# Optimization experiments

Hardware: AMD Instinct MI355X
Metric: run time of the kernel (lower is better)

The kernel has to match this reference:

```python
import jax, jax.numpy as jnp
import numpy as np

EPS = 1e-5

def _layernorm(x, g, b):
    mu = jnp.mean(x, axis=-1, keepdims=True)
    var = jnp.mean(jnp.square(x - mu), axis=-1, keepdims=True)
    return (x - mu) * jax.lax.rsqrt(var + EPS) * g + b

def _silu(x):
    return x * jax.nn.sigmoid(x)

def _xavier(key, shape):
    fan_out, fan_in = shape
    limit = np.sqrt(6.0 / (fan_in + fan_out))
    return jax.random.uniform(key, shape, jnp.float32, -limit, limit)

def setup_inputs() -> dict:
    key = jax.random.key(0)
    ks = jax.random.split(key, 4)
    B = 2097152
    return {
        'x': jax.random.normal(ks[0], (B, 24), jnp.float32),
        'w1': _xavier(ks[1], (64, 24)), 'b1': jnp.zeros((64,), jnp.float32),
        'g1': jnp.ones((64,), jnp.float32), 'be1': jnp.zeros((64,), jnp.float32),
        'w2': _xavier(ks[2], (64, 64)), 'b2': jnp.zeros((64,), jnp.float32),
        'g2': jnp.ones((64,), jnp.float32), 'be2': jnp.zeros((64,), jnp.float32),
        'w3': _xavier(ks[3], (7, 64)), 'b3': jnp.zeros((7,), jnp.float32),
        'g3': jnp.ones((7,), jnp.float32), 'be3': jnp.zeros((7,), jnp.float32),
    }

def reference(x, w1, b1, g1, be1, w2, b2, g2, be2, w3, b3, g3, be3):
    h = _silu(_layernorm(x @ w1.T + b1, g1, be1))      # [B, 64]
    h = _silu(_layernorm(h @ w2.T + b2, g2, be2))      # [B, 64]
    h = _layernorm(h @ w3.T + b3, g3, be3)             # [B, 7]
    return jax.nn.softmax(h, axis=-1)
```

## Files before the change

kernel.cpp:

```cpp
#include <hip/hip_runtime.h>
#include <math.h>

#define BLOCK 256
#define WPB 4
#define NBLOCKS 2048

typedef float  f32x4 __attribute__((ext_vector_type(4)));
typedef float  f32x2 __attribute__((ext_vector_type(2)));
typedef short  short8 __attribute__((ext_vector_type(8)));
typedef unsigned int u32;
typedef u32 u32x4 __attribute__((ext_vector_type(4)));
typedef u32 u32x2 __attribute__((ext_vector_type(2)));

static __device__ __forceinline__ f32x4 mfma16(short8 a, short8 b, f32x4 c) {
    return __builtin_amdgcn_mfma_f32_16x16x32_bf16(a, b, c, 0, 0, 0);
}

static __device__ __forceinline__ f32x4 zero4() { f32x4 z = {0.f, 0.f, 0.f, 0.f}; return z; }

static __device__ __forceinline__ u32 cvt_pk(float lo, float hi) {
    u32 r;
    asm("v_cvt_pk_bf16_f32 %0, %1, %2" : "=v"(r) : "v"(lo), "v"(hi));
    return r;
}
static __device__ __forceinline__ float unpk_lo(u32 p) { return __builtin_bit_cast(float, p << 16); }
static __device__ __forceinline__ float unpk_hi(u32 p) { return __builtin_bit_cast(float, p & 0xffff0000u); }

static __device__ __forceinline__ short8 mk_frag(u32 a, u32 b, u32 c, u32 d) {
    u32x4 t = {a, b, c, d};
    return __builtin_bit_cast(short8, t);
}

struct Frag2 { short8 hi, lo; };

static __device__ __forceinline__ Frag2 split8(f32x4 a, f32x4 b) {
    u32 h0 = cvt_pk(a[0], a[1]), h1 = cvt_pk(a[2], a[3]);
    u32 h2 = cvt_pk(b[0], b[1]), h3 = cvt_pk(b[2], b[3]);
    u32 l0 = cvt_pk(a[0] - unpk_lo(h0), a[1] - unpk_hi(h0));
    u32 l1 = cvt_pk(a[2] - unpk_lo(h1), a[3] - unpk_hi(h1));
    u32 l2 = cvt_pk(b[0] - unpk_lo(h2), b[1] - unpk_hi(h2));
    u32 l3 = cvt_pk(b[2] - unpk_lo(h3), b[3] - unpk_hi(h3));
    Frag2 r; r.hi = mk_frag(h0, h1, h2, h3); r.lo = mk_frag(l0, l1, l2, l3);
    return r;
}

static __device__ __forceinline__ void split4(f32x4 v, u32x2& hi, u32x2& lo) {
    u32 h0 = cvt_pk(v[0], v[1]), h1 = cvt_pk(v[2], v[3]);
    u32 l0 = cvt_pk(v[0] - unpk_lo(h0), v[1] - unpk_hi(h0));
    u32 l1 = cvt_pk(v[2] - unpk_lo(h1), v[3] - unpk_hi(h1));
    hi = u32x2{h0, h1}; lo = u32x2{l0, l1};
}

static __device__ __forceinline__ Frag2 wfrag(const float* p) {
    return split8(*(const f32x4*)p, *(const f32x4*)(p + 4));
}

static __device__ __forceinline__ float red4(float v) {
    v += __shfl_xor(v, 16);
    v += __shfl_xor(v, 32);
    return v;
}
static __device__ __forceinline__ float redmax4(float v) {
    v = fmaxf(v, __shfl_xor(v, 16));
    v = fmaxf(v, __shfl_xor(v, 32));
    return v;
}

struct TState {
    f32x4 xa, xb;
    f32x4 d[4];
    short8 bhHi[2], bhLo[2];
    f32x4 d3;
};

static __device__ __forceinline__ void ph_l1(TState& t, const Frag2& bx, const Frag2* w1f) {
#pragma unroll
    for (int mt = 0; mt < 4; ++mt) {
        f32x4 d = mfma16(w1f[mt].hi, bx.hi, zero4());
        d = mfma16(w1f[mt].hi, bx.lo, d);
        d = mfma16(w1f[mt].lo, bx.hi, d);
        t.d[mt] = d;
    }
}

static __device__ __forceinline__ void ph_l2_lds(TState& t,
        const unsigned char* sW2h, const unsigned char* sW2l, u32 crow, u32 ch, int q) {
    const u32 r0 = crow + ((((u32)q) ^ ch) << 4);
    const u32 r1 = crow + ((((u32)(4 + q)) ^ ch) << 4);
#pragma unroll
    for (int mt = 0; mt < 4; ++mt) {
        const u32 mo = (u32)mt * 2048u;
        short8 h0 = *(const short8*)(sW2h + mo + r0);
        short8 h1 = *(const short8*)(sW2h + mo + r1);
        short8 l0 = *(const short8*)(sW2l + mo + r0);
        short8 l1 = *(const short8*)(sW2l + mo + r1);
        f32x4 d = mfma16(h0, t.bhHi[0], zero4());
        d = mfma16(h0, t.bhLo[0], d);
        d = mfma16(l0, t.bhHi[0], d);
        d = mfma16(h1, t.bhHi[1], d);
        d = mfma16(h1, t.bhLo[1], d);
        d = mfma16(l1, t.bhHi[1], d);
        t.d[mt] = d;
    }
}

static __device__ __forceinline__ void ph_l3(TState& t, const Frag2* w3f) {
    f32x4 a = mfma16(w3f[0].hi, t.bhHi[0], zero4());
    a = mfma16(w3f[0].hi, t.bhLo[0], a);
    a = mfma16(w3f[0].lo, t.bhHi[0], a);
    f32x4 b = mfma16(w3f[1].hi, t.bhHi[1], zero4());
    b = mfma16(w3f[1].hi, t.bhLo[1], b);
    b = mfma16(w3f[1].lo, t.bhHi[1], b);
#pragma unroll
    for (int r = 0; r < 4; ++r) t.d3[r] = a[r] + b[r];
}

template<int PB, int PG, int PBE>
static __device__ __forceinline__ void ph_ln_silu(TState& t, const float* sP, int q) {
    float s = 0.f, s2 = 0.f;
#pragma unroll
    for (int mt = 0; mt < 4; ++mt) {
        if (PB >= 0) {
            const f32x4 bv = *(const f32x4*)(sP + PB + mt * 16 + q * 4);
#pragma unroll
            for (int r = 0; r < 4; ++r) t.d[mt][r] += bv[r];
        }
#pragma unroll
        for (int r = 0; r < 4; ++r) { float v = t.d[mt][r]; s += v; s2 = fmaf(v, v, s2); }
    }
    s = red4(s); s2 = red4(s2);
    const float mu = s * (1.f / 64.f);
    const float var = s2 * (1.f / 64.f) - mu * mu;
    const float inv = __builtin_amdgcn_rsqf(var + 1e-5f);
    const float cns = -mu * inv;
#pragma unroll
    for (int mt = 0; mt < 4; ++mt) {
        const f32x4 gv  = *(const f32x4*)(sP + PG  + mt * 16 + q * 4);
        const f32x4 bev = *(const f32x4*)(sP + PBE + mt * 16 + q * 4);
#pragma unroll
        for (int r = 0; r < 4; ++r) {
            float tt = fmaf(t.d[mt][r], inv, cns);
            float v  = fmaf(tt, gv[r], bev[r]);
            t.d[mt][r] = v * __builtin_amdgcn_rcpf(1.f + __expf(-v));
        }
    }
}

static __device__ __forceinline__ void ph_stage(TState& t, unsigned char* sHi, unsigned char* sLo,
                                                u32 crow, u32 ch, int q) {
#pragma unroll
    for (int mt = 0; mt < 4; ++mt) {
        u32x2 hi, lo;
        split4(t.d[mt], hi, lo);
        u32 off = crow + ((((u32)(mt * 2 + (q >> 1))) ^ ch) << 4) + (u32)((q & 1) * 8);
        *(u32x2*)(sHi + off) = hi;
        *(u32x2*)(sLo + off) = lo;
    }
#pragma unroll
    for (int kk = 0; kk < 2; ++kk) {
        u32 roff = crow + ((((u32)(kk * 4 + q)) ^ ch) << 4);
        t.bhHi[kk] = *(const short8*)(sHi + roff);
        t.bhLo[kk] = *(const short8*)(sLo + roff);
    }
}

static __device__ __forceinline__ void ph_out(TState& t, const float* sP, int q, int c, int lane,
                                              unsigned char* ob, float* out, int tile,
                                              int oc0, int of0, int oc1, int of1) {
    const f32x4 b3v  = *(const f32x4*)(sP + 384 + q * 4);
    const f32x4 g3v  = *(const f32x4*)(sP + 400 + q * 4);
    const f32x4 be3v = *(const f32x4*)(sP + 416 + q * 4);
    f32x4 d3 = t.d3;
    float s = 0.f, s2 = 0.f;
#pragma unroll
    for (int r = 0; r < 4; ++r) {
        float v = d3[r] + b3v[r];
        d3[r] = v;
        const bool ok = (q * 4 + r) < 7;
        if (ok) { s += v; s2 = fmaf(v, v, s2); }
    }
    s = red4(s); s2 = red4(s2);
    const float mu = s * (1.f / 7.f);
    const float var = s2 * (1.f / 7.f) - mu * mu;
    const float inv = __builtin_amdgcn_rsqf(var + 1e-5f);
    const float cns = -mu * inv;

    float z[4]; float mx = -1e30f;
#pragma unroll
    for (int r = 0; r < 4; ++r) {
        z[r] = fmaf(fmaf(d3[r], inv, cns), g3v[r], be3v[r]);
        const bool ok = (q * 4 + r) < 7;
        if (ok) mx = fmaxf(mx, z[r]);
    }
    mx = redmax4(mx);
    float es = 0.f; float e[4];
#pragma unroll
    for (int r = 0; r < 4; ++r) {
        const bool ok = (q * 4 + r) < 7;
        e[r] = ok ? __expf(z[r] - mx) : 0.f;
        es += e[r];
    }
    es = red4(es);
    const float rs = __builtin_amdgcn_rcpf(es);

    if (q == 0) {
        f32x4 v = {e[0] * rs, e[1] * rs, e[2] * rs, e[3] * rs};
        *(f32x4*)(ob + c * 48) = v;
    } else if (q == 1) {
        f32x2 v = {e[0] * rs, e[1] * rs};
        *(f32x2*)(ob + c * 48 + 16) = v;
        *(float*)(ob + c * 48 + 24) = e[2] * rs;
    }
    float* outp = out + (size_t)tile * 112;
    outp[lane] = *(const float*)(ob + oc0 * 48 + of0 * 4);
    if (lane < 48) outp[64 + lane] = *(const float*)(ob + oc1 * 48 + of1 * 4);
}

__global__ __launch_bounds__(BLOCK, 3) void mlp_mfma4_kernel(
    const float* __restrict__ x,
    const float* __restrict__ w1, const float* __restrict__ b1,
    const float* __restrict__ g1, const float* __restrict__ be1,
    const float* __restrict__ w2, const float* __restrict__ b2,
    const float* __restrict__ g2, const float* __restrict__ be2,
    const float* __restrict__ w3, const float* __restrict__ b3,
    const float* __restrict__ g3, const float* __restrict__ be3,
    float* __restrict__ out, int ntiles)
{
    __shared__ __align__(16) unsigned char smem[WPB * 4096 + 16384];
    __shared__ __align__(16) float sP[6 * 64 + 3 * 16];

    const int tid = threadIdx.x;
    const int lane = tid & 63;
    const int wib  = tid >> 6;
    const int c = lane & 15;
    const int q = lane >> 4;

    unsigned char* wb   = smem + wib * 4096;
    unsigned char* sHi  = wb;
    unsigned char* sLo  = wb + 2048;
    unsigned char* ob   = sHi;
    unsigned char* sW2h = smem + WPB * 4096;
    unsigned char* sW2l = sW2h + 8192;

    for (int i = tid; i < 512; i += BLOCK) {
        const int row = i >> 3, cb = i & 7;
        Frag2 f = wfrag(w2 + row * 64 + cb * 8);
        const u32 off = (u32)row * 128u + (u32)((cb ^ (row & 7)) << 4);
        *(short8*)(sW2h + off) = f.hi;
        *(short8*)(sW2l + off) = f.lo;
    }
    if (tid < 64) {
        sP[        tid] = b1[tid];  sP[ 64 + tid] = g1[tid];  sP[128 + tid] = be1[tid];
        sP[192 + tid] = b2[tid];    sP[256 + tid] = g2[tid];  sP[320 + tid] = be2[tid];
    }
    if (tid < 16) {
        const bool ok = tid < 7;
        sP[384 + tid] = ok ? b3[tid]  : 0.f;
        sP[400 + tid] = ok ? g3[tid]  : 0.f;
        sP[416 + tid] = ok ? be3[tid] : 0.f;
    }

    const u32 crow = (u32)c * 128u;
    const u32 ch   = (u32)(c & 7);

    Frag2 w1f[4];
#pragma unroll
    for (int mt = 0; mt < 4; ++mt) {
        if (q < 3) {
            w1f[mt] = wfrag(w1 + (mt * 16 + c) * 24 + q * 8);
        } else {
            float s = b1[mt * 16 + c];
            f32x4 a = {s, 0.f, 0.f, 0.f};
            w1f[mt] = split8(a, zero4());
        }
    }
    Frag2 w3f[2];
#pragma unroll
    for (int kk = 0; kk < 2; ++kk) {
        if (c < 7) w3f[kk] = wfrag(w3 + c * 64 + kk * 32 + q * 8);
        else       { w3f[kk].hi = mk_frag(0,0,0,0); w3f[kk].lo = mk_frag(0,0,0,0); }
    }

    __syncthreads();

    const int oc0 = lane / 7, of0 = lane - oc0 * 7;
    const int i1 = lane + 64;
    const int oc1 = i1 / 7, of1 = i1 - oc1 * 7;

    const int wid = blockIdx.x * WPB + wib;
    const int ts  = gridDim.x * WPB;

    TState A;
    A.xa = zero4(); A.xb = zero4();
    if (wid < ntiles && q < 3) {
        const float* xp = x + ((size_t)wid * 16 + c) * 24 + q * 8;
        A.xa = *(const f32x4*)xp; A.xb = *(const f32x4*)(xp + 4);
    }
    if (q == 3) A.xa[0] = 1.0f;

    for (int tile = wid; tile < ntiles; tile += ts) {
        asm volatile("" ::: "memory");

        Frag2 bx = split8(A.xa, A.xb);

        {
            const int nt = tile + ts;
            if (nt < ntiles && q < 3) {
                const float* xp = x + ((size_t)nt * 16 + c) * 24 + q * 8;
                A.xa = *(const f32x4*)xp; A.xb = *(const f32x4*)(xp + 4);
            }
        }

        ph_l1(A, bx, w1f);
        ph_ln_silu<-1, 64, 128>(A, sP, q);
        ph_stage(A, sHi, sLo, crow, ch, q);
        ph_l2_lds(A, sW2h, sW2l, crow, ch, q);
        ph_ln_silu<192, 256, 320>(A, sP, q);
        ph_stage(A, sHi, sLo, crow, ch, q);
        ph_l3(A, w3f);
        ph_out(A, sP, q, c, lane, ob, out, tile, oc0, of0, oc1, of1);
    }
}

extern "C" void kernel_launch(void* const* d_in, const int* in_sizes, int n_in,
                              void* d_out, int out_size, void* d_ws, size_t ws_size,
                              hipStream_t stream) {
    const float* x   = (const float*)d_in[0];
    const float* w1  = (const float*)d_in[1];
    const float* b1  = (const float*)d_in[2];
    const float* g1  = (const float*)d_in[3];
    const float* be1 = (const float*)d_in[4];
    const float* w2  = (const float*)d_in[5];
    const float* b2  = (const float*)d_in[6];
    const float* g2  = (const float*)d_in[7];
    const float* be2 = (const float*)d_in[8];
    const float* w3  = (const float*)d_in[9];
    const float* b3  = (const float*)d_in[10];
    const float* g3  = (const float*)d_in[11];
    const float* be3 = (const float*)d_in[12];
    float* out = (float*)d_out;

    const int B = in_sizes[0] / 24;
    const int ntiles = B / 16;
    hipLaunchKernelGGL(mlp_mfma4_kernel, dim3(NBLOCKS), dim3(BLOCK), 0, stream,
                       x, w1, b1, g1, be1, w2, b2, g2, be2, w3, b3, g3, be3,
                       out, ntiles);
}
```

Before: 190.0 us.

## Move W3 fragments to LDS and raise occupancy target to four blocks per CU

The layer-3 weight fragments were held in registers for the whole persistent loop. They are now stored in a swizzled LDS buffer and reloaded every tile, which frees VGPRs so the launch bound can go from 3 to 4 blocks per CU. The LayerNorm and softmax math is also rewritten as vector f32x4 operations with a tree reduction. The cost is extra LDS reads per tile and 4 KB more shared memory per block, and forcing the tighter register budget could cause spills.

```diff
diff --git a/kernel.cpp b/kernel.cpp
--- a/kernel.cpp
+++ b/kernel.cpp
@@ -104,30 +104,37 @@
     }
 }
 
-static __device__ __forceinline__ void ph_l3(TState& t, const Frag2* w3f) {
-    f32x4 a = mfma16(w3f[0].hi, t.bhHi[0], zero4());
-    a = mfma16(w3f[0].hi, t.bhLo[0], a);
-    a = mfma16(w3f[0].lo, t.bhHi[0], a);
-    f32x4 b = mfma16(w3f[1].hi, t.bhHi[1], zero4());
-    b = mfma16(w3f[1].hi, t.bhLo[1], b);
-    b = mfma16(w3f[1].lo, t.bhHi[1], b);
-#pragma unroll
-    for (int r = 0; r < 4; ++r) t.d3[r] = a[r] + b[r];
+static __device__ __forceinline__ void ph_l3_lds(TState& t,
+        const unsigned char* sW3h, const unsigned char* sW3l, u32 crow, u32 ch, int q) {
+    const u32 r0 = crow + ((((u32)q) ^ ch) << 4);
+    const u32 r1 = crow + ((((u32)(4 + q)) ^ ch) << 4);
+    short8 h0 = *(const short8*)(sW3h + r0);
+    short8 h1 = *(const short8*)(sW3h + r1);
+    short8 l0 = *(const short8*)(sW3l + r0);
+    short8 l1 = *(const short8*)(sW3l + r1);
+    f32x4 a = mfma16(h0, t.bhHi[0], zero4());
+    a = mfma16(h0, t.bhLo[0], a);
+    a = mfma16(l0, t.bhHi[0], a);
+    f32x4 b = mfma16(h1, t.bhHi[1], zero4());
+    b = mfma16(h1, t.bhLo[1], b);
+    b = mfma16(l1, t.bhHi[1], b);
+    t.d3 = a + b;
 }
 
 template<int PB, int PG, int PBE>
 static __device__ __forceinline__ void ph_ln_silu(TState& t, const float* sP, int q) {
-    float s = 0.f, s2 = 0.f;
-#pragma unroll
-    for (int mt = 0; mt < 4; ++mt) {
-        if (PB >= 0) {
-            const f32x4 bv = *(const f32x4*)(sP + PB + mt * 16 + q * 4);
-#pragma unroll
-            for (int r = 0; r < 4; ++r) t.d[mt][r] += bv[r];
-        }
-#pragma unroll
-        for (int r = 0; r < 4; ++r) { float v = t.d[mt][r]; s += v; s2 = fmaf(v, v, s2); }
-    }
+    if (PB >= 0) {
+#pragma unroll
+        for (int mt = 0; mt < 4; ++mt)
+            t.d[mt] += *(const f32x4*)(sP + PB + mt * 16 + q * 4);
+    }
+    f32x4 acc  = (t.d[0] + t.d[1]) + (t.d[2] + t.d[3]);
+    f32x4 acc2 = t.d[0] * t.d[0];
+    acc2 += t.d[1] * t.d[1];
+    acc2 += t.d[2] * t.d[2];
+    acc2 += t.d[3] * t.d[3];
+    float s  = (acc[0] + acc[1]) + (acc[2] + acc[3]);
+    float s2 = (acc2[0] + acc2[1]) + (acc2[2] + acc2[3]);
     s = red4(s); s2 = red4(s2);
     const float mu = s * (1.f / 64.f);
     const float var = s2 * (1.f / 64.f) - mu * mu;
@@ -137,12 +144,13 @@
     for (int mt = 0; mt < 4; ++mt) {
         const f32x4 gv  = *(const f32x4*)(sP + PG  + mt * 16 + q * 4);
         const f32x4 bev = *(const f32x4*)(sP + PBE + mt * 16 + q * 4);
-#pragma unroll
-        for (int r = 0; r < 4; ++r) {
-            float tt = fmaf(t.d[mt][r], inv, cns);
-            float v  = fmaf(tt, gv[r], bev[r]);
-            t.d[mt][r] = v * __builtin_amdgcn_rcpf(1.f + __expf(-v));
-        }
+        f32x4 tt = t.d[mt] * inv + cns;
+        f32x4 v  = tt * gv + bev;
+        f32x4 sg;
+#pragma unroll
+        for (int r = 0; r < 4; ++r)
+            sg[r] = __builtin_amdgcn_rcpf(1.f + __expf(-v[r]));
+        t.d[mt] = v * sg;
     }
 }
 
@@ -170,14 +178,12 @@
     const f32x4 b3v  = *(const f32x4*)(sP + 384 + q * 4);
     const f32x4 g3v  = *(const f32x4*)(sP + 400 + q * 4);
     const f32x4 be3v = *(const f32x4*)(sP + 416 + q * 4);
-    f32x4 d3 = t.d3;
+    f32x4 d3 = t.d3 + b3v;
     float s = 0.f, s2 = 0.f;
 #pragma unroll
     for (int r = 0; r < 4; ++r) {
-        float v = d3[r] + b3v[r];
-        d3[r] = v;
         const bool ok = (q * 4 + r) < 7;
-        if (ok) { s += v; s2 = fmaf(v, v, s2); }
+        if (ok) { s += d3[r]; s2 = fmaf(d3[r], d3[r], s2); }
     }
     s = red4(s); s2 = red4(s2);
     const float mu = s * (1.f / 7.f);
@@ -185,10 +191,10 @@
     const float inv = __builtin_amdgcn_rsqf(var + 1e-5f);
     const float cns = -mu * inv;
 
-    float z[4]; float mx = -1e30f;
+    f32x4 z = (d3 * inv + cns) * g3v + be3v;
+    float mx = -1e30f;
 #pragma unroll
     for (int r = 0; r < 4; ++r) {
-        z[r] = fmaf(fmaf(d3[r], inv, cns), g3v[r], be3v[r]);
         const bool ok = (q * 4 + r) < 7;
         if (ok) mx = fmaxf(mx, z[r]);
     }
@@ -216,7 +222,7 @@
     if (lane < 48) outp[64 + lane] = *(const float*)(ob + oc1 * 48 + of1 * 4);
 }
 
-__global__ __launch_bounds__(BLOCK, 3) void mlp_mfma4_kernel(
+__global__ __launch_bounds__(BLOCK, 4) void mlp_mfma5_kernel(
     const float* __restrict__ x,
     const float* __restrict__ w1, const float* __restrict__ b1,
     const float* __restrict__ g1, const float* __restrict__ be1,
@@ -226,7 +232,7 @@
     const float* __restrict__ g3, const float* __restrict__ be3,
     float* __restrict__ out, int ntiles)
 {
-    __shared__ __align__(16) unsigned char smem[WPB * 4096 + 16384];
+    __shared__ __align__(16) unsigned char smem[WPB * 4096 + 16384 + 4096];
     __shared__ __align__(16) float sP[6 * 64 + 3 * 16];
 
     const int tid = threadIdx.x;
@@ -241,6 +247,8 @@
     unsigned char* ob   = sHi;
     unsigned char* sW2h = smem + WPB * 4096;
     unsigned char* sW2l = sW2h + 8192;
+    unsigned char* sW3h = sW2l + 8192;
+    unsigned char* sW3l = sW3h + 2048;
 
     for (int i = tid; i < 512; i += BLOCK) {
         const int row = i >> 3, cb = i & 7;
@@ -248,6 +256,15 @@
         const u32 off = (u32)row * 128u + (u32)((cb ^ (row & 7)) << 4);
         *(short8*)(sW2h + off) = f.hi;
         *(short8*)(sW2l + off) = f.lo;
+    }
+    if (tid < 128) {
+        const int row = tid >> 3, cb = tid & 7;
+        Frag2 f;
+        if (row < 7) f = wfrag(w3 + row * 64 + cb * 8);
+        else         { f.hi = mk_frag(0,0,0,0); f.lo = mk_frag(0,0,0,0); }
+        const u32 off = (u32)row * 128u + (u32)((cb ^ (row & 7)) << 4);
+        *(short8*)(sW3h + off) = f.hi;
+        *(short8*)(sW3l + off) = f.lo;
     }
     if (tid < 64) {
         sP[        tid] = b1[tid];  sP[ 64 + tid] = g1[tid];  sP[128 + tid] = be1[tid];
@@ -274,12 +291,6 @@
             w1f[mt] = split8(a, zero4());
         }
     }
-    Frag2 w3f[2];
-#pragma unroll
-    for (int kk = 0; kk < 2; ++kk) {
-        if (c < 7) w3f[kk] = wfrag(w3 + c * 64 + kk * 32 + q * 8);
-        else       { w3f[kk].hi = mk_frag(0,0,0,0); w3f[kk].lo = mk_frag(0,0,0,0); }
-    }
 
     __syncthreads();
 
@@ -317,7 +328,7 @@
         ph_l2_lds(A, sW2h, sW2l, crow, ch, q);
         ph_ln_silu<192, 256, 320>(A, sP, q);
         ph_stage(A, sHi, sLo, crow, ch, q);
-        ph_l3(A, w3f);
+        ph_l3_lds(A, sW3h, sW3l, crow, ch, q);
         ph_out(A, sP, q, c, lane, ob, out, tile, oc0, of0, oc1, of1);
     }
 }
@@ -342,7 +353,7 @@
 
     const int B = in_sizes[0] / 24;
     const int ntiles = B / 16;
-    hipLaunchKernelGGL(mlp_mfma4_kernel, dim3(NBLOCKS), dim3(BLOCK), 0, stream,
+    hipLaunchKernelGGL(mlp_mfma5_kernel, dim3(NBLOCKS), dim3(BLOCK), 0, stream,
                        x, w1, b1, g1, be1, w2, b2, g2, be2, w3, b3, g3, be3,
                        out, ntiles);
 }
```

Result: faster. 183.5 us (-3.4%).

## Halve per-wave LDS staging and raise occupancy target with vectorized LN math

Applied to the files above, without the earlier changes.

Staging now uses a single 2KB per-wave LDS buffer: hi bf16 parts are written and read first, then the lo parts reuse the same space. This halves LDS per block. Launch bounds go from 3 to 6 blocks per CU and the grid shrinks to 1536 blocks. LayerNorm, SiLU and the output math are rewritten with f32x4 vector ops and tree reductions. The aim is more resident waves to hide latency, at the cost of tighter register budgets and possible spills, plus extra serialization inside the staging step.

```diff
diff --git a/kernel.cpp b/kernel.cpp
--- a/kernel.cpp
+++ b/kernel.cpp
@@ -3,7 +3,7 @@
 
 #define BLOCK 256
 #define WPB 4
-#define NBLOCKS 2048
+#define NBLOCKS 1536
 
 typedef float  f32x4 __attribute__((ext_vector_type(4)));
 typedef float  f32x2 __attribute__((ext_vector_type(2)));
@@ -111,23 +111,23 @@
     f32x4 b = mfma16(w3f[1].hi, t.bhHi[1], zero4());
     b = mfma16(w3f[1].hi, t.bhLo[1], b);
     b = mfma16(w3f[1].lo, t.bhHi[1], b);
-#pragma unroll
-    for (int r = 0; r < 4; ++r) t.d3[r] = a[r] + b[r];
+    t.d3 = a + b;
 }
 
 template<int PB, int PG, int PBE>
 static __device__ __forceinline__ void ph_ln_silu(TState& t, const float* sP, int q) {
-    float s = 0.f, s2 = 0.f;
-#pragma unroll
-    for (int mt = 0; mt < 4; ++mt) {
-        if (PB >= 0) {
-            const f32x4 bv = *(const f32x4*)(sP + PB + mt * 16 + q * 4);
-#pragma unroll
-            for (int r = 0; r < 4; ++r) t.d[mt][r] += bv[r];
-        }
-#pragma unroll
-        for (int r = 0; r < 4; ++r) { float v = t.d[mt][r]; s += v; s2 = fmaf(v, v, s2); }
-    }
+    if (PB >= 0) {
+#pragma unroll
+        for (int mt = 0; mt < 4; ++mt)
+            t.d[mt] += *(const f32x4*)(sP + PB + mt * 16 + q * 4);
+    }
+    f32x4 acc  = (t.d[0] + t.d[1]) + (t.d[2] + t.d[3]);
+    f32x4 acc2 = t.d[0] * t.d[0];
+    acc2 += t.d[1] * t.d[1];
+    acc2 += t.d[2] * t.d[2];
+    acc2 += t.d[3] * t.d[3];
+    float s  = (acc[0] + acc[1]) + (acc[2] + acc[3]);
+    float s2 = (acc2[0] + acc2[1]) + (acc2[2] + acc2[3]);
     s = red4(s); s2 = red4(s2);
     const float mu = s * (1.f / 64.f);
     const float var = s2 * (1.f / 64.f) - mu * mu;
@@ -137,30 +137,40 @@
     for (int mt = 0; mt < 4; ++mt) {
         const f32x4 gv  = *(const f32x4*)(sP + PG  + mt * 16 + q * 4);
         const f32x4 bev = *(const f32x4*)(sP + PBE + mt * 16 + q * 4);
-#pragma unroll
-        for (int r = 0; r < 4; ++r) {
-            float tt = fmaf(t.d[mt][r], inv, cns);
-            float v  = fmaf(tt, gv[r], bev[r]);
-            t.d[mt][r] = v * __builtin_amdgcn_rcpf(1.f + __expf(-v));
-        }
-    }
-}
-
-static __device__ __forceinline__ void ph_stage(TState& t, unsigned char* sHi, unsigned char* sLo,
+        f32x4 tt = t.d[mt] * inv + cns;
+        f32x4 v  = tt * gv + bev;
+        f32x4 sg;
+#pragma unroll
+        for (int r = 0; r < 4; ++r)
+            sg[r] = __builtin_amdgcn_rcpf(1.f + __expf(-v[r]));
+        t.d[mt] = v * sg;
+    }
+}
+
+static __device__ __forceinline__ void ph_stage(TState& t, unsigned char* sS,
                                                 u32 crow, u32 ch, int q) {
-#pragma unroll
-    for (int mt = 0; mt < 4; ++mt) {
-        u32x2 hi, lo;
-        split4(t.d[mt], hi, lo);
+    u32x2 hiv[4], lov[4];
+#pragma unroll
+    for (int mt = 0; mt < 4; ++mt) split4(t.d[mt], hiv[mt], lov[mt]);
+#pragma unroll
+    for (int mt = 0; mt < 4; ++mt) {
         u32 off = crow + ((((u32)(mt * 2 + (q >> 1))) ^ ch) << 4) + (u32)((q & 1) * 8);
-        *(u32x2*)(sHi + off) = hi;
-        *(u32x2*)(sLo + off) = lo;
+        *(u32x2*)(sS + off) = hiv[mt];
     }
 #pragma unroll
     for (int kk = 0; kk < 2; ++kk) {
         u32 roff = crow + ((((u32)(kk * 4 + q)) ^ ch) << 4);
-        t.bhHi[kk] = *(const short8*)(sHi + roff);
-        t.bhLo[kk] = *(const short8*)(sLo + roff);
+        t.bhHi[kk] = *(const short8*)(sS + roff);
+    }
+#pragma unroll
+    for (int mt = 0; mt < 4; ++mt) {
+        u32 off = crow + ((((u32)(mt * 2 + (q >> 1))) ^ ch) << 4) + (u32)((q & 1) * 8);
+        *(u32x2*)(sS + off) = lov[mt];
+    }
+#pragma unroll
+    for (int kk = 0; kk < 2; ++kk) {
+        u32 roff = crow + ((((u32)(kk * 4 + q)) ^ ch) << 4);
+        t.bhLo[kk] = *(const short8*)(sS + roff);
     }
 }
 
@@ -170,14 +180,12 @@
     const f32x4 b3v  = *(const f32x4*)(sP + 384 + q * 4);
     const f32x4 g3v  = *(const f32x4*)(sP + 400 + q * 4);
     const f32x4 be3v = *(const f32x4*)(sP + 416 + q * 4);
-    f32x4 d3 = t.d3;
+    f32x4 d3 = t.d3 + b3v;
     float s = 0.f, s2 = 0.f;
 #pragma unroll
     for (int r = 0; r < 4; ++r) {
-        float v = d3[r] + b3v[r];
-        d3[r] = v;
         const bool ok = (q * 4 + r) < 7;
-        if (ok) { s += v; s2 = fmaf(v, v, s2); }
+        if (ok) { s += d3[r]; s2 = fmaf(d3[r], d3[r], s2); }
     }
     s = red4(s); s2 = red4(s2);
     const float mu = s * (1.f / 7.f);
@@ -185,10 +193,10 @@
     const float inv = __builtin_amdgcn_rsqf(var + 1e-5f);
     const float cns = -mu * inv;
 
-    float z[4]; float mx = -1e30f;
+    f32x4 z = (d3 * inv + cns) * g3v + be3v;
+    float mx = -1e30f;
 #pragma unroll
     for (int r = 0; r < 4; ++r) {
-        z[r] = fmaf(fmaf(d3[r], inv, cns), g3v[r], be3v[r]);
         const bool ok = (q * 4 + r) < 7;
         if (ok) mx = fmaxf(mx, z[r]);
     }
@@ -216,7 +224,7 @@
     if (lane < 48) outp[64 + lane] = *(const float*)(ob + oc1 * 48 + of1 * 4);
 }
 
-__global__ __launch_bounds__(BLOCK, 3) void mlp_mfma4_kernel(
+__global__ __launch_bounds__(BLOCK, 6) void mlp_mfma8_kernel(
     const float* __restrict__ x,
     const float* __restrict__ w1, const float* __restrict__ b1,
     const float* __restrict__ g1, const float* __restrict__ be1,
@@ -226,7 +234,7 @@
     const float* __restrict__ g3, const float* __restrict__ be3,
     float* __restrict__ out, int ntiles)
 {
-    __shared__ __align__(16) unsigned char smem[WPB * 4096 + 16384];
+    __shared__ __align__(16) unsigned char smem[WPB * 2048 + 16384];
     __shared__ __align__(16) float sP[6 * 64 + 3 * 16];
 
     const int tid = threadIdx.x;
@@ -235,11 +243,9 @@
     const int c = lane & 15;
     const int q = lane >> 4;
 
-    unsigned char* wb   = smem + wib * 4096;
-    unsigned char* sHi  = wb;
-    unsigned char* sLo  = wb + 2048;
-    unsigned char* ob   = sHi;
-    unsigned char* sW2h = smem + WPB * 4096;
+    unsigned char* sS   = smem + wib * 2048;
+    unsigned char* ob   = sS;
+    unsigned char* sW2h = smem + WPB * 2048;
     unsigned char* sW2l = sW2h + 8192;
 
     for (int i = tid; i < 512; i += BLOCK) {
@@ -313,10 +319,10 @@
 
         ph_l1(A, bx, w1f);
         ph_ln_silu<-1, 64, 128>(A, sP, q);
-        ph_stage(A, sHi, sLo, crow, ch, q);
+        ph_stage(A, sS, crow, ch, q);
         ph_l2_lds(A, sW2h, sW2l, crow, ch, q);
         ph_ln_silu<192, 256, 320>(A, sP, q);
-        ph_stage(A, sHi, sLo, crow, ch, q);
+        ph_stage(A, sS, crow, ch, q);
         ph_l3(A, w3f);
         ph_out(A, sP, q, c, lane, ob, out, tile, oc0, of0, oc1, of1);
     }
@@ -341,8 +347,8 @@
     float* out = (float*)d_out;
 
     const int B = in_sizes[0] / 24;
-    const int ntiles = B / 16;
-    hipLaunchKernelGGL(mlp_mfma4_kernel, dim3(NBLOCKS), dim3(BLOCK), 0, stream,
+    const int nt = B / 16;
+    hipLaunchKernelGGL(mlp_mfma8_kernel, dim3(NBLOCKS), dim3(BLOCK), 0, stream,
                        x, w1, b1, g1, be1, w2, b2, g2, be2, w3, b3, g3, be3,
-                       out, ntiles);
-}
+                       out, nt);
+}
```

Result: slower. 263.1 us (+38.5%).
